# Kernel optimization log

Measured on AMD Instinct MI355X. Metric: run time of the kernel, lower is better.

Reference implementation:

```python
import jax, jax.numpy as jnp
import numpy as np

B, C, H, W = 8, 512, 32, 32
N_HEADS, HEAD_DIM = 8, 64
EPS = 1e-5


def _layernorm(x, g, b):
    mu = jnp.mean(x, axis=-1, keepdims=True)
    var = jnp.mean(jnp.square(x - mu), axis=-1, keepdims=True)
    return (x - mu) * jax.lax.rsqrt(var + EPS) * g + b


def setup_inputs() -> dict:
    key = jax.random.key(0)
    ks = jax.random.split(key, 16)
    u = lambda k, shp: jax.random.uniform(k, shp, dtype=jnp.float32)
    inp = {
        "x": jax.random.normal(ks[0], (B, C, H, W), dtype=jnp.float32),
        "t": jax.random.normal(ks[1], (B,), dtype=jnp.float32),
        # attention params (torch.rand init in source)
        "K_W": u(ks[2], (N_HEADS, C, HEAD_DIM)), "K_b": u(ks[3], (N_HEADS, HEAD_DIM)),
        "Q_W": u(ks[4], (N_HEADS, C, HEAD_DIM)), "Q_b": u(ks[5], (N_HEADS, HEAD_DIM)),
        "V_W": u(ks[6], (N_HEADS, C, HEAD_DIM)), "V_b": u(ks[7], (N_HEADS, HEAD_DIM)),
        "O_W": u(ks[8], (N_HEADS, HEAD_DIM, C)), "O_b": u(ks[9], (C,)),
        # pre-attention LayerNorm
        "ln1_g": jnp.ones((C,), jnp.float32), "ln1_b": jnp.zeros((C,), jnp.float32),
        # MLP: LayerNorm -> Linear -> GELU -> Linear
        "ln2_g": jnp.ones((C,), jnp.float32), "ln2_b": jnp.zeros((C,), jnp.float32),
        "W1": jax.random.normal(ks[10], (C, C), dtype=jnp.float32) / np.sqrt(C),
        "b1": jnp.zeros((C,), jnp.float32),
        "W2": jax.random.normal(ks[11], (C, C), dtype=jnp.float32) / np.sqrt(C),
        "b2": jnp.zeros((C,), jnp.float32),
    }
    return inp


def reference(x, t, K_W, K_b, Q_W, Q_b, V_W, V_b, O_W, O_b,
              ln1_g, ln1_b, ln2_g, ln2_b, W1, b1, W2, b2):
    b, c, h, w = x.shape
    xs = x.reshape(b, c, h * w).transpose(0, 2, 1)           # b s c
    res = _layernorm(xs, ln1_g, ln1_b)
    q = jnp.einsum('bsc,ncd->bsnd', res, Q_W) + Q_b          # b s n_h h_dim
    k = jnp.einsum('bsc,ncd->bsnd', res, K_W) + K_b
    v = jnp.einsum('bsc,ncd->bsnd', res, V_W) + V_b
    scores = jnp.einsum('bsnd,btnd->bnst', q, k) / jnp.sqrt(jnp.float32(c))
    attn = jax.nn.softmax(scores, axis=-1)                   # b n_h s s
    o = jnp.einsum('bnst,btnd->bsnd', attn, v)
    out = jnp.einsum('bsnd,ndc->bsc', o, O_W) + O_b
    out = out + xs                                           # residual
    m = _layernorm(out, ln2_g, ln2_b)
    m = jax.nn.gelu(m @ W1 + b1, approximate=False) @ W2 + b2
    out = m + out
    return out.transpose(0, 2, 1).reshape(b, c, h, w)
```

## Files before the change

### kernel.cpp

```cpp
#include <hip/hip_runtime.h>
#include <math.h>

#define BB 8
#define CC 512
#define SS 1024
#define NHH 8
#define HDD 64
#define KD 512

typedef __attribute__((ext_vector_type(8))) short short8;
typedef __attribute__((ext_vector_type(4))) float f32x4;
typedef __attribute__((ext_vector_type(4))) unsigned short ushort4v;
typedef __attribute__((ext_vector_type(2))) unsigned int u32x2;

__device__ __forceinline__ unsigned short f2bf(float x) {
  union { float f; unsigned int u; } c; c.f = x;
  unsigned int r = (c.u + 0x7FFFu + ((c.u >> 16) & 1u)) >> 16;
  return (unsigned short)r;
}
__device__ __forceinline__ float b2f(unsigned short h) {
  union { unsigned int u; float f; } c; c.u = ((unsigned int)h) << 16; return c.f;
}

#define GLD_LDS(gp, lp) __builtin_amdgcn_global_load_lds( \
    (const __attribute__((address_space(1))) void*)(gp),  \
    (__attribute__((address_space(3))) void*)(lp), 16, 0, 0)

__device__ __forceinline__ float block_reduce_sum(float v) {
  __shared__ float sm[4];
  #pragma unroll
  for (int o = 32; o > 0; o >>= 1) v += __shfl_down(v, o, 64);
  if ((threadIdx.x & 63) == 0) sm[threadIdx.x >> 6] = v;
  __syncthreads();
  float r = (sm[0] + sm[1]) + (sm[2] + sm[3]);
  __syncthreads();
  return r;
}

__global__ __launch_bounds__(256) void ln1_apply(
    const float* __restrict__ x, const float2* __restrict__ mustd,
    const float* __restrict__ g, const float* __restrict__ be,
    unsigned short* __restrict__ yh, unsigned short* __restrict__ yl,
    unsigned short* __restrict__ xh, unsigned short* __restrict__ xl) {
  __shared__ float tile[32][33];
  const int b = blockIdx.z, c0 = blockIdx.y * 32, s0 = blockIdx.x * 32;
  const int tx = threadIdx.x, ty = threadIdx.y;
  const float* xb = x + ((size_t)b * CC + c0) * SS + s0;
  #pragma unroll
  for (int i = ty; i < 32; i += 8)
    tile[i][tx] = xb[(size_t)i * SS + tx];
  __syncthreads();
  const float gc = g[c0 + tx], bc = be[c0 + tx];
  #pragma unroll
  for (int i = ty; i < 32; i += 8) {
    const float2 ms = mustd[b * SS + s0 + i];
    const float v = tile[tx][i];
    const float y = (v - ms.x) * ms.y * gc + bc;
    const size_t oi = ((size_t)b * SS + s0 + i) * CC + c0 + tx;
    const unsigned short hy = f2bf(y);
    yh[oi] = hy; yl[oi] = f2bf(y - b2f(hy));
    const unsigned short hx = f2bf(v);
    xh[oi] = hx; xl[oi] = f2bf(v - b2f(hx));
  }
}

__global__ __launch_bounds__(256) void ln_bf16_k(const float* __restrict__ in,
                                                 const float* __restrict__ g,
                                                 const float* __restrict__ be,
                                                 unsigned short* __restrict__ outh) {
  size_t row = blockIdx.x;
  const float* r = in + row * CC;
  int t = threadIdx.x;
  float v0 = r[t], v1 = r[t + 256];
  float s = block_reduce_sum(v0 + v1);
  float mu = s * (1.0f / CC);
  float d0 = v0 - mu, d1 = v1 - mu;
  float vs = block_reduce_sum(d0 * d0 + d1 * d1);
  float rstd = rsqrtf(vs * (1.0f / CC) + 1e-5f);
  outh[row * CC + t]       = f2bf(d0 * rstd * g[t] + be[t]);
  outh[row * CC + t + 256] = f2bf(d1 * rstd * g[t + 256] + be[t + 256]);
}

__global__ __launch_bounds__(256) void convert_and_stats(
    const float* __restrict__ QW, const float* __restrict__ KW,
    const float* __restrict__ VW, const float* __restrict__ OW,
    const float* __restrict__ W1, const float* __restrict__ W2,
    const float* __restrict__ Qb, const float* __restrict__ Kb,
    const float* __restrict__ Vb,
    unsigned short* __restrict__ BtQKh, unsigned short* __restrict__ BtQKl,
    unsigned short* __restrict__ BtVh,
    unsigned short* __restrict__ BtOh, unsigned short* __restrict__ BtOl,
    unsigned short* __restrict__ BtW1h, unsigned short* __restrict__ BtW2h,
    float* __restrict__ qkvb,
    const float* __restrict__ x, float2* __restrict__ mustd) {
  const int bid = blockIdx.x;
  if (bid < 1536) {
    const float SCL = 0.044194173824159216f * 1.4426950408889634f;
    __shared__ float tile[32][33];
    const int bx = bid & 15, by = (bid >> 4) & 1, p = bid >> 5;
    const int wsel = p >> 3, sub = p & 7;
    const int k0 = bx * 32, d0 = by * 32;
    const int tx = threadIdx.x & 31, ty = threadIdx.x >> 5;
    const float* w; int rs; unsigned short *dh, *dl; int nbase; float mul = 1.0f;
    switch (wsel) {
      case 0:  w = QW + sub * 32768; rs = 64;  dh = BtQKh; dl = BtQKl;  nbase = sub * 64; mul = SCL; break;
      case 1:  w = KW + sub * 32768; rs = 64;  dh = BtQKh; dl = BtQKl;  nbase = 512 + sub * 64;  break;
      case 2:  w = VW + sub * 32768; rs = 64;  dh = BtVh;  dl = nullptr; nbase = sub * 64;       break;
      case 3:  w = OW + sub * 64;    rs = 512; dh = BtOh;  dl = BtOl;   nbase = sub * 64;        break;
      case 4:  w = W1 + sub * 64;    rs = 512; dh = BtW1h; dl = nullptr; nbase = sub * 64;       break;
      default: w = W2 + sub * 64;    rs = 512; dh = BtW2h; dl = nullptr; nbase = sub * 64;       break;
    }
    for (int i = ty; i < 32; i += 8)
      tile[i][tx] = w[(size_t)(k0 + i) * rs + d0 + tx];
    __syncthreads();
    for (int i = ty; i < 32; i += 8) {
      float f = tile[tx][i] * mul;
      unsigned short h = f2bf(f);
      size_t idx = (size_t)(nbase + d0 + i) * KD + k0 + tx;
      dh[idx] = h;
      if (dl) dl[idx] = f2bf(f - b2f(h));
    }
    if (bid == 0) {
      int t = threadIdx.x;
      for (int i = t; i < 1536; i += 256)
        qkvb[i] = i < 512 ? Qb[i] * SCL : (i < 1024 ? Kb[i - 512] : Vb[i - 1024]);
    }
  } else {
    const int bid2 = bid - 1536;
    const int b = bid2 >> 4, s0 = (bid2 & 15) * 64;
    const int sl = threadIdx.x & 63, cg = threadIdx.x >> 6;
    const float* xp = x + (size_t)b * CC * SS + s0 + sl;
    float ps = 0.f, pq = 0.f;
    #pragma unroll 8
    for (int i = 0; i < 128; ++i) {
      const float v = xp[(size_t)(cg * 128 + i) * SS];
      ps += v; pq += v * v;
    }
    __shared__ float sred[2][4][64];
    sred[0][cg][sl] = ps; sred[1][cg][sl] = pq;
    __syncthreads();
    if (cg == 0) {
      const float s = (sred[0][0][sl] + sred[0][1][sl]) + (sred[0][2][sl] + sred[0][3][sl]);
      const float q = (sred[1][0][sl] + sred[1][1][sl]) + (sred[1][2][sl] + sred[1][3][sl]);
      const float mu = s * (1.0f / CC);
      const float rs = rsqrtf(q * (1.0f / CC) - mu * mu + 1e-5f);
      mustd[b * SS + s0 + sl] = make_float2(mu, rs);
    }
  }
}

__global__ __launch_bounds__(256) void gemm_qkv(
    const unsigned short* __restrict__ Ah, const unsigned short* __restrict__ Al,
    const unsigned short* __restrict__ Bth, const unsigned short* __restrict__ Btl,
    const float* __restrict__ bias,
    unsigned short* __restrict__ qkh, unsigned short* __restrict__ qkl,
    unsigned short* __restrict__ vt) {
  __shared__ __align__(16) unsigned short smem[4 * 128 * 32];
  unsigned short* As = smem;
  unsigned short* Bs = smem + 2 * 128 * 32;
  const int tid = threadIdx.x;
  const int w = tid >> 6, l = tid & 63, quad = l >> 4, lm = l & 15;
  const int f = blockIdx.x, xcd = f & 7, gidx = f >> 3;
  const int n0 = (gidx >> 3) * 128;
  const int m0 = (((gidx & 7) << 3) | xcd) * 128;
  const bool splitB = n0 < 1024;
  const int wm = (w >> 1) * 64, wn = (w & 1) * 64;
  const int srow = tid >> 2;
  const int sch = (((tid & 3) ^ (srow & 3)) * 8);
  const unsigned short* Agh = Ah + (size_t)(m0 + srow) * KD + sch;
  const unsigned short* Agl = Al + (size_t)(m0 + srow) * KD + sch;
  const unsigned short* Bgh = Bth + (size_t)(n0 + srow) * KD + sch;
  const unsigned short* Bgl = Btl + (size_t)(n0 + srow) * KD + sch;
  unsigned short* Aswh = As + w * 512;
  unsigned short* Aswl = As + 4096 + w * 512;
  unsigned short* Bswh = Bs + w * 512;
  unsigned short* Bswl = Bs + 4096 + w * 512;
  const int rch = ((quad ^ (lm & 3)) * 8);
  const f32x4 fzero = {0.f, 0.f, 0.f, 0.f};
  f32x4 acc[4][4];
  #pragma unroll
  for (int i = 0; i < 4; ++i)
    #pragma unroll
    for (int j = 0; j < 4; ++j) acc[i][j] = fzero;
  for (int k0 = 0; k0 < KD; k0 += 32) {
    __syncthreads();
    GLD_LDS(Agh + k0, Aswh);
    GLD_LDS(Agh + k0 + 64 * KD, Aswh + 2048);
    GLD_LDS(Agl + k0, Aswl);
    GLD_LDS(Agl + k0 + 64 * KD, Aswl + 2048);
    GLD_LDS(Bgh + k0, Bswh);
    GLD_LDS(Bgh + k0 + 64 * KD, Bswh + 2048);
    if (splitB) {
      GLD_LDS(Bgl + k0, Bswl);
      GLD_LDS(Bgl + k0 + 64 * KD, Bswl + 2048);
    }
    __syncthreads();
    short8 afh[4], afl[4], bfh[4], bfl[4];
    #pragma unroll
    for (int i = 0; i < 4; ++i) {
      afh[i] = *(const short8*)(As + (wm + i * 16 + lm) * 32 + rch);
      afl[i] = *(const short8*)(As + 4096 + (wm + i * 16 + lm) * 32 + rch);
    }
    #pragma unroll
    for (int j = 0; j < 4; ++j)
      bfh[j] = *(const short8*)(Bs + (wn + j * 16 + lm) * 32 + rch);
    if (splitB) {
      #pragma unroll
      for (int j = 0; j < 4; ++j)
        bfl[j] = *(const short8*)(Bs + 4096 + (wn + j * 16 + lm) * 32 + rch);
      #pragma unroll
      for (int i = 0; i < 4; ++i)
        #pragma unroll
        for (int j = 0; j < 4; ++j) {
          f32x4 t = acc[i][j];
          t = __builtin_amdgcn_mfma_f32_16x16x32_bf16(afh[i], bfh[j], t, 0, 0, 0);
          t = __builtin_amdgcn_mfma_f32_16x16x32_bf16(afh[i], bfl[j], t, 0, 0, 0);
          t = __builtin_amdgcn_mfma_f32_16x16x32_bf16(afl[i], bfh[j], t, 0, 0, 0);
          acc[i][j] = t;
        }
    } else {
      #pragma unroll
      for (int i = 0; i < 4; ++i)
        #pragma unroll
        for (int j = 0; j < 4; ++j)
          acc[i][j] = __builtin_amdgcn_mfma_f32_16x16x32_bf16(afh[i], bfh[j], acc[i][j], 0, 0, 0);
    }
  }
  if (splitB) {
    #pragma unroll
    for (int i = 0; i < 4; ++i) {
      const int row = m0 + wm + i * 16 + quad * 4;
      #pragma unroll
      for (int j = 0; j < 4; ++j) {
        const int ncol = n0 + wn + j * 16 + lm;
        const float bv = bias[ncol];
        #pragma unroll
        for (int r = 0; r < 4; ++r) {
          const float xv = acc[i][j][r] + bv;
          const size_t oi = (size_t)(row + r) * 1024 + ncol;
          unsigned short h = f2bf(xv);
          qkh[oi] = h;
          qkl[oi] = f2bf(xv - b2f(h));
        }
      }
    }
  } else {
    __syncthreads();
    #pragma unroll
    for (int i = 0; i < 4; ++i) {
      const int mlb = wm + i * 16 + quad * 4;
      #pragma unroll
      for (int j = 0; j < 4; ++j) {
        const int nl = wn + j * 16 + lm;
        const float bv = bias[n0 + nl];
        ushort4v pk;
        #pragma unroll
        for (int r = 0; r < 4; ++r) pk[r] = f2bf(acc[i][j][r] + bv);
        const int chunk = ((mlb >> 3) ^ (nl & 15));
        *(ushort4v*)(smem + nl * 128 + chunk * 8 + (mlb & 7)) = pk;
      }
    }
    __syncthreads();
    const int tn = tid >> 4, tc = tid & 15;
    const int bb2 = m0 >> 10, sbase = m0 & 1023;
    #pragma unroll
    for (int pass = 0; pass < 8; ++pass) {
      const int nl = pass * 16 + tn;
      const int hh = (n0 - 1024 + nl) >> 6, dd = nl & 63;
      short8 v8 = *(const short8*)(smem + nl * 128 + ((tc ^ (nl & 15)) * 8));
      *(short8*)(vt + ((size_t)(bb2 * 8 + hh) * 64 + dd) * 1024 + sbase + tc * 8) = v8;
    }
  }
}

template<int SB, int GELU, int OUTMODE, int RESID, int TRANS>
__global__ __launch_bounds__(256) void gemm64(
    const unsigned short* __restrict__ Ah,
    const unsigned short* __restrict__ Bh, const unsigned short* __restrict__ Bl,
    const float* __restrict__ bias, const float* __restrict__ residf,
    const unsigned short* __restrict__ residh, const unsigned short* __restrict__ residl,
    unsigned short* __restrict__ outh, float* __restrict__ outf, int ldc) {
  constexpr int STAGE = (SB ? 3 : 2) * 8192;
  constexpr int TSIZE = TRANS ? 64 * 65 * 4 : 0;
  __shared__ __align__(16) unsigned char smem[STAGE > TSIZE ? STAGE : TSIZE];
  unsigned short* As  = (unsigned short*)smem;
  unsigned short* Bs  = (unsigned short*)(smem + 8192);
  unsigned short* Bls = (unsigned short*)(smem + 16384);
  float (*ttile)[65]  = (float(*)[65])smem;
  const int tid = threadIdx.x;
  const int w = tid >> 6, l = tid & 63, quad = l >> 4, lm = l & 15;
  const int f = blockIdx.x, xcd = f & 7, gidx = f >> 3;
  const int n0 = (gidx >> 4) * 64;
  const int m0 = (((gidx & 15) << 3) | xcd) * 64;
  const int wm = (w >> 1) * 32, wn = (w & 1) * 32;
  const int srow8 = tid >> 3;
  const int sch8  = ((tid & 7) ^ (srow8 & 7)) * 8;
  const unsigned short* Ag  = Ah + (size_t)(m0 + srow8) * KD + sch8;
  const unsigned short* Bg  = Bh + (size_t)(n0 + srow8) * KD + sch8;
  const unsigned short* Bgl = SB ? Bl + (size_t)(n0 + srow8) * KD + sch8 : nullptr;
  const f32x4 fzero = {0.f, 0.f, 0.f, 0.f};
  f32x4 acc[2][2];
  #pragma unroll
  for (int i = 0; i < 2; ++i)
    #pragma unroll
    for (int j = 0; j < 2; ++j) acc[i][j] = fzero;
  for (int k0 = 0; k0 < KD; k0 += 64) {
    __syncthreads();
    GLD_LDS(Ag + k0, As + w * 512);
    GLD_LDS(Ag + k0 + 32 * KD, As + 2048 + w * 512);
    GLD_LDS(Bg + k0, Bs + w * 512);
    GLD_LDS(Bg + k0 + 32 * KD, Bs + 2048 + w * 512);
    if constexpr (SB) {
      GLD_LDS(Bgl + k0, Bls + w * 512);
      GLD_LDS(Bgl + k0 + 32 * KD, Bls + 2048 + w * 512);
    }
    __syncthreads();
    #pragma unroll
    for (int ks = 0; ks < 2; ++ks) {
      const int kc = ((ks * 4 + quad) ^ (lm & 7)) * 8;
      short8 af[2], bfh[2], bfl[2];
      #pragma unroll
      for (int i = 0; i < 2; ++i)
        af[i] = *(const short8*)(As + (wm + i * 16 + lm) * 64 + kc);
      #pragma unroll
      for (int j = 0; j < 2; ++j)
        bfh[j] = *(const short8*)(Bs + (wn + j * 16 + lm) * 64 + kc);
      if constexpr (SB) {
        #pragma unroll
        for (int j = 0; j < 2; ++j)
          bfl[j] = *(const short8*)(Bls + (wn + j * 16 + lm) * 64 + kc);
      }
      #pragma unroll
      for (int i = 0; i < 2; ++i)
        #pragma unroll
        for (int j = 0; j < 2; ++j) {
          f32x4 t = acc[i][j];
          t = __builtin_amdgcn_mfma_f32_16x16x32_bf16(af[i], bfh[j], t, 0, 0, 0);
          if constexpr (SB)
            t = __builtin_amdgcn_mfma_f32_16x16x32_bf16(af[i], bfl[j], t, 0, 0, 0);
          acc[i][j] = t;
        }
    }
  }
  if constexpr (TRANS) __syncthreads();
  #pragma unroll
  for (int i = 0; i < 2; ++i) {
    const int row = m0 + wm + i * 16 + quad * 4;
    #pragma unroll
    for (int j = 0; j < 2; ++j) {
      const int col = n0 + wn + j * 16 + lm;
      const float bv = bias[col];
      #pragma unroll
      for (int r = 0; r < 4; ++r) {
        float x = acc[i][j][r] + bv;
        if (GELU) x = 0.5f * x * (1.0f + erff(x * 0.70710678118654752f));
        const size_t ri = (size_t)(row + r) * CC + col;
        if (RESID == 1) x += residf[ri];
        if (RESID == 2) x += b2f(residh[ri]) + b2f(residl[ri]);
        if constexpr (TRANS) {
          ttile[wm + i * 16 + quad * 4 + r][wn + j * 16 + lm] = x;
        } else {
          const size_t oi = (size_t)(row + r) * ldc + col;
          if (OUTMODE == 0) outf[oi] = x;
          else outh[oi] = f2bf(x);
        }
      }
    }
  }
  if constexpr (TRANS) {
    __syncthreads();
    const int bi = m0 >> 10, s0 = m0 & 1023;
    const int s = tid & 63;
    #pragma unroll
    for (int c0 = 0; c0 < 64; c0 += 4) {
      const int col = c0 + (tid >> 6);
      outf[(size_t)(bi * 512 + n0 + col) * 1024 + s0 + s] = ttile[s][col];
    }
  }
}

__global__ __launch_bounds__(256) void attn_mfma(
    const unsigned short* __restrict__ QKh, const unsigned short* __restrict__ QKl,
    const unsigned short* __restrict__ Vt, unsigned short* __restrict__ Oh) {
  __shared__ __align__(16) unsigned short Ksh[64 * 64], Ksl[64 * 64];
  __shared__ __align__(16) unsigned short Vts[64 * 64];
  __shared__ __align__(16) unsigned short Pts[4][16 * 64];
  const int f = blockIdx.x, xcd = f & 7, gidx = f >> 3;
  const int bh = (xcd << 3) | (gidx >> 4);
  const int q0 = (gidx & 15) * 64, h = bh & 7, b = bh >> 3;
  const int tid = threadIdx.x, w = tid >> 6, l = tid & 63, quad = l >> 4, lm = l & 15;
  const int LDQ = 2 * CC;
  const size_t qkbase = (size_t)b * SS * LDQ;
  const int srow8 = tid >> 3;
  const int sch8  = ((tid & 7) ^ (srow8 & 7)) * 8;
  const unsigned short* Vg = Vt + ((size_t)(b * 8 + h) * 64 + srow8) * 1024 + sch8;
  short8 qh[2], ql[2];
  {
    const size_t qo = qkbase + (size_t)(q0 + w * 16 + lm) * LDQ + h * 64 + quad * 8;
    qh[0] = *(const short8*)(QKh + qo);
    qh[1] = *(const short8*)(QKh + qo + 32);
    ql[0] = *(const short8*)(QKl + qo);
    ql[1] = *(const short8*)(QKl + qo + 32);
  }
  const f32x4 fzero = {0.f, 0.f, 0.f, 0.f};
  float m = -1e30f, lsum = 0.f;
  f32x4 oacc[4];
  #pragma unroll
  for (int j = 0; j < 4; ++j) oacc[j] = fzero;
  unsigned char* Pb = (unsigned char*)(Pts[w]);
  const int pwbase = lm * 128 + ((quad & 1) << 3);
  const int prbase = lm * 128;
  for (int kt = 0; kt < SS; kt += 64) {
    __syncthreads();
    {
      const unsigned short* kg  = QKh + qkbase + (size_t)(kt + srow8) * LDQ + CC + h * 64 + sch8;
      const unsigned short* kgl = QKl + qkbase + (size_t)(kt + srow8) * LDQ + CC + h * 64 + sch8;
      GLD_LDS(kg, Ksh + w * 512);
      GLD_LDS(kg + 32 * LDQ, Ksh + 2048 + w * 512);
      GLD_LDS(kgl, Ksl + w * 512);
      GLD_LDS(kgl + 32 * LDQ, Ksl + 2048 + w * 512);
      GLD_LDS(Vg + kt, Vts + w * 512);
      GLD_LDS(Vg + kt + 32 * 1024, Vts + 2048 + w * 512);
    }
    __syncthreads();
    f32x4 sc[4];
    {
      const int kc = (quad ^ (lm & 7)) * 8;
      #pragma unroll
      for (int j = 0; j < 4; ++j) {
        short8 kh = *(const short8*)(Ksh + (j * 16 + lm) * 64 + kc);
        short8 kl = *(const short8*)(Ksl + (j * 16 + lm) * 64 + kc);
        f32x4 t = __builtin_amdgcn_mfma_f32_16x16x32_bf16(kh, qh[0], fzero, 0, 0, 0);
        t = __builtin_amdgcn_mfma_f32_16x16x32_bf16(kl, qh[0], t, 0, 0, 0);
        t = __builtin_amdgcn_mfma_f32_16x16x32_bf16(kh, ql[0], t, 0, 0, 0);
        sc[j] = t;
      }
    }
    {
      const int kc = ((4 + quad) ^ (lm & 7)) * 8;
      #pragma unroll
      for (int j = 0; j < 4; ++j) {
        short8 kh = *(const short8*)(Ksh + (j * 16 + lm) * 64 + kc);
        short8 kl = *(const short8*)(Ksl + (j * 16 + lm) * 64 + kc);
        f32x4 t = sc[j];
        t = __builtin_amdgcn_mfma_f32_16x16x32_bf16(kh, qh[1], t, 0, 0, 0);
        t = __builtin_amdgcn_mfma_f32_16x16x32_bf16(kl, qh[1], t, 0, 0, 0);
        t = __builtin_amdgcn_mfma_f32_16x16x32_bf16(kh, ql[1], t, 0, 0, 0);
        sc[j] = t;
      }
    }
    float mt0 = fmaxf(fmaxf(sc[0][0], sc[0][1]), fmaxf(sc[0][2], sc[0][3]));
    float mt1 = fmaxf(fmaxf(sc[1][0], sc[1][1]), fmaxf(sc[1][2], sc[1][3]));
    float mt2 = fmaxf(fmaxf(sc[2][0], sc[2][1]), fmaxf(sc[2][2], sc[2][3]));
    float mt3 = fmaxf(fmaxf(sc[3][0], sc[3][1]), fmaxf(sc[3][2], sc[3][3]));
    float mt = fmaxf(fmaxf(mt0, mt1), fmaxf(mt2, mt3));
    mt = fmaxf(mt, __shfl_xor(mt, 16, 64));
    mt = fmaxf(mt, __shfl_xor(mt, 32, 64));
    const float mnew = fmaxf(m, mt);
    if (__any(mnew > m)) {
      const float alpha = exp2f(m - mnew);
      m = mnew;
      lsum *= alpha;
      #pragma unroll
      for (int j = 0; j < 4; ++j)
        #pragma unroll
        for (int r = 0; r < 4; ++r) oacc[j][r] *= alpha;
    }
    float ls = 0.f;
    #pragma unroll
    for (int j = 0; j < 4; ++j)
      #pragma unroll
      for (int r = 0; r < 4; ++r) {
        sc[j][r] = exp2f(sc[j][r] - m);
        ls += sc[j][r];
      }
    ls += __shfl_xor(ls, 16, 64);
    ls += __shfl_xor(ls, 32, 64);
    lsum += ls;
    #pragma unroll
    for (int j = 0; j < 4; ++j) {
      union { float f; unsigned int u; } c0, c1, c2, c3;
      c0.f = sc[j][0]; c1.f = sc[j][1]; c2.f = sc[j][2]; c3.f = sc[j][3];
      u32x2 pk;
      pk[0] = __builtin_amdgcn_perm(c1.u, c0.u, 0x07060302u);
      pk[1] = __builtin_amdgcn_perm(c3.u, c2.u, 0x07060302u);
      const int slot = ((j << 1) | (quad >> 1)) ^ (lm & 7);
      *(u32x2*)(Pb + pwbase + (slot << 4)) = pk;
    }
    #pragma unroll
    for (int st = 0; st < 2; ++st) {
      short8 pf = *(const short8*)(Pb + prbase + ((((st << 2) | quad) ^ (lm & 7)) << 4));
      const int kc = ((st * 4 + quad) ^ (lm & 7)) * 8;
      #pragma unroll
      for (int j = 0; j < 4; ++j) {
        short8 vv = *(const short8*)(Vts + (j * 16 + lm) * 64 + kc);
        oacc[j] = __builtin_amdgcn_mfma_f32_16x16x32_bf16(vv, pf, oacc[j], 0, 0, 0);
      }
    }
  }
  const float inv = 1.f / lsum;
  const size_t obase =
      (size_t)b * SS * CC + (size_t)(q0 + w * 16 + lm) * CC + h * 64 + quad * 4;
  #pragma unroll
  for (int j = 0; j < 4; ++j) {
    ushort4v pk;
    #pragma unroll
    for (int r = 0; r < 4; ++r) pk[r] = f2bf(oacc[j][r] * inv);
    *(ushort4v*)(Oh + obase + j * 16) = pk;
  }
}

extern "C" void kernel_launch(void* const* d_in, const int* in_sizes, int n_in,
                              void* d_out, int out_size, void* d_ws, size_t ws_size,
                              hipStream_t stream) {
  const float* x    = (const float*)d_in[0];
  const float* K_W  = (const float*)d_in[2];
  const float* K_b  = (const float*)d_in[3];
  const float* Q_W  = (const float*)d_in[4];
  const float* Q_b  = (const float*)d_in[5];
  const float* V_W  = (const float*)d_in[6];
  const float* V_b  = (const float*)d_in[7];
  const float* O_W  = (const float*)d_in[8];
  const float* O_b  = (const float*)d_in[9];
  const float* ln1g = (const float*)d_in[10];
  const float* ln1b = (const float*)d_in[11];
  const float* ln2g = (const float*)d_in[12];
  const float* ln2b = (const float*)d_in[13];
  const float* W1   = (const float*)d_in[14];
  const float* b1   = (const float*)d_in[15];
  const float* W2   = (const float*)d_in[16];
  const float* b2   = (const float*)d_in[17];
  float* out = (float*)d_out;

  unsigned char* ws = (unsigned char*)d_ws;
  const size_t MB = 1u << 20;
  unsigned short* qkh   = (unsigned short*)(ws);
  unsigned short* qkl   = (unsigned short*)(ws + 16 * MB);
  unsigned short* vt    = (unsigned short*)(ws + 32 * MB);
  unsigned short* ln1h  = (unsigned short*)(ws + 40 * MB);
  unsigned short* ln1l  = (unsigned short*)(ws + 48 * MB);
  unsigned short* xsh   = (unsigned short*)(ws + 56 * MB);
  unsigned short* xsl   = (unsigned short*)(ws + 64 * MB);
  unsigned short* oh    = ln1h;
  float* out1           = (float*)(ws + 72 * MB);
  unsigned short* ln2h  = qkh;
  unsigned short* geluh = (unsigned short*)(ws + 8 * MB);
  unsigned short* BtAll = (unsigned short*)(ws + 88 * MB);
  unsigned short* BtQKh = BtAll;
  unsigned short* BtVh  = BtAll + 1024 * 512;
  unsigned short* BtQKl = BtVh + 512 * 512;
  unsigned short* BtOh  = BtQKl + 1024 * 512;
  unsigned short* BtOl  = BtOh + 512 * 512;
  unsigned short* BtW1h = BtOl + 512 * 512;
  unsigned short* BtW2h = BtW1h + 512 * 512;
  float* qkvb           = (float*)(BtW2h + 512 * 512);
  float2* mustd         = (float2*)(ws + 96 * MB);

  dim3 tb32(32, 8);
  convert_and_stats<<<1536 + 128, 256, 0, stream>>>(
      Q_W, K_W, V_W, O_W, W1, W2, Q_b, K_b, V_b,
      BtQKh, BtQKl, BtVh, BtOh, BtOl, BtW1h, BtW2h, qkvb, x, mustd);
  ln1_apply<<<dim3(SS / 32, CC / 32, BB), tb32, 0, stream>>>(
      x, mustd, ln1g, ln1b, ln1h, ln1l, xsh, xsl);
  gemm_qkv<<<768, 256, 0, stream>>>(
      ln1h, ln1l, BtAll, BtQKl, qkvb, qkh, qkl, vt);
  attn_mfma<<<1024, 256, 0, stream>>>(qkh, qkl, vt, oh);
  gemm64<1, 0, 0, 2, 0><<<1024, 256, 0, stream>>>(
      oh, BtOh, BtOl, O_b, nullptr, xsh, xsl, nullptr, out1, CC);
  ln_bf16_k<<<BB * SS, 256, 0, stream>>>(out1, ln2g, ln2b, ln2h);
  gemm64<0, 1, 1, 0, 0><<<1024, 256, 0, stream>>>(
      ln2h, BtW1h, nullptr, b1, nullptr, nullptr, nullptr, geluh, nullptr, CC);
  gemm64<0, 0, 0, 1, 1><<<1024, 256, 0, stream>>>(
      geluh, BtW2h, nullptr, b2, out1, nullptr, nullptr, nullptr, out, CC);
}
```

Before: 264.3 us.

## Register-prefetch next K/V tile in attention loop and raise MFMA priority

The attention kernel used direct global-to-LDS loads, with each K/V tile loaded and waited on before compute. It now loads the next tile into registers during the current tile's compute and writes them to LDS at the start of the next iteration, overlapping global latency with the MFMA work. The MFMA sections are also wrapped in s_setprio(1)/(0) to favour matrix issue across waves. This costs extra VGPRs, which may lower occupancy, and adds a register-to-LDS store pass in place of the direct LDS load path.

```diff
diff --git a/kernel.cpp b/kernel.cpp
--- a/kernel.cpp
+++ b/kernel.cpp
@@ -393,7 +393,10 @@
   const size_t qkbase = (size_t)b * SS * LDQ;
   const int srow8 = tid >> 3;
   const int sch8  = ((tid & 7) ^ (srow8 & 7)) * 8;
-  const unsigned short* Vg = Vt + ((size_t)(b * 8 + h) * 64 + srow8) * 1024 + sch8;
+  const unsigned short* Vg  = Vt + ((size_t)(b * 8 + h) * 64 + srow8) * 1024 + sch8;
+  const unsigned short* kgh = QKh + qkbase + (size_t)srow8 * LDQ + CC + h * 64 + sch8;
+  const unsigned short* kgl = QKl + qkbase + (size_t)srow8 * LDQ + CC + h * 64 + sch8;
+  const int lofs = w * 512 + l * 8;
   short8 qh[2], ql[2];
   {
     const size_t qo = qkbase + (size_t)(q0 + w * 16 + lm) * LDQ + h * 64 + quad * 8;
@@ -410,20 +413,32 @@
   unsigned char* Pb = (unsigned char*)(Pts[w]);
   const int pwbase = lm * 128 + ((quad & 1) << 3);
   const int prbase = lm * 128;
+  short8 s0h = *(const short8*)(kgh);
+  short8 s1h = *(const short8*)(kgh + (size_t)32 * LDQ);
+  short8 s0l = *(const short8*)(kgl);
+  short8 s1l = *(const short8*)(kgl + (size_t)32 * LDQ);
+  short8 s0v = *(const short8*)(Vg);
+  short8 s1v = *(const short8*)(Vg + 32 * 1024);
   for (int kt = 0; kt < SS; kt += 64) {
     __syncthreads();
+    *(short8*)(Ksh + lofs)        = s0h;
+    *(short8*)(Ksh + 2048 + lofs) = s1h;
+    *(short8*)(Ksl + lofs)        = s0l;
+    *(short8*)(Ksl + 2048 + lofs) = s1l;
+    *(short8*)(Vts + lofs)        = s0v;
+    *(short8*)(Vts + 2048 + lofs) = s1v;
+    __syncthreads();
     {
-      const unsigned short* kg  = QKh + qkbase + (size_t)(kt + srow8) * LDQ + CC + h * 64 + sch8;
-      const unsigned short* kgl = QKl + qkbase + (size_t)(kt + srow8) * LDQ + CC + h * 64 + sch8;
-      GLD_LDS(kg, Ksh + w * 512);
-      GLD_LDS(kg + 32 * LDQ, Ksh + 2048 + w * 512);
-      GLD_LDS(kgl, Ksl + w * 512);
-      GLD_LDS(kgl + 32 * LDQ, Ksl + 2048 + w * 512);
-      GLD_LDS(Vg + kt, Vts + w * 512);
-      GLD_LDS(Vg + kt + 32 * 1024, Vts + 2048 + w * 512);
-    }
-    __syncthreads();
+      const int ktn = (kt + 64) & (SS - 1);
+      s0h = *(const short8*)(kgh + (size_t)ktn * LDQ);
+      s1h = *(const short8*)(kgh + (size_t)(ktn + 32) * LDQ);
+      s0l = *(const short8*)(kgl + (size_t)ktn * LDQ);
+      s1l = *(const short8*)(kgl + (size_t)(ktn + 32) * LDQ);
+      s0v = *(const short8*)(Vg + ktn);
+      s1v = *(const short8*)(Vg + ktn + 32 * 1024);
+    }
     f32x4 sc[4];
+    __builtin_amdgcn_s_setprio(1);
     {
       const int kc = (quad ^ (lm & 7)) * 8;
       #pragma unroll
@@ -449,6 +464,7 @@
         sc[j] = t;
       }
     }
+    __builtin_amdgcn_s_setprio(0);
     float mt0 = fmaxf(fmaxf(sc[0][0], sc[0][1]), fmaxf(sc[0][2], sc[0][3]));
     float mt1 = fmaxf(fmaxf(sc[1][0], sc[1][1]), fmaxf(sc[1][2], sc[1][3]));
     float mt2 = fmaxf(fmaxf(sc[2][0], sc[2][1]), fmaxf(sc[2][2], sc[2][3]));
@@ -487,6 +503,7 @@
       const int slot = ((j << 1) | (quad >> 1)) ^ (lm & 7);
       *(u32x2*)(Pb + pwbase + (slot << 4)) = pk;
     }
+    __builtin_amdgcn_s_setprio(1);
     #pragma unroll
     for (int st = 0; st < 2; ++st) {
       short8 pf = *(const short8*)(Pb + prbase + ((((st << 2) | quad) ^ (lm & 7)) << 4));
@@ -497,6 +514,7 @@
         oacc[j] = __builtin_amdgcn_mfma_f32_16x16x32_bf16(vv, pf, oacc[j], 0, 0, 0);
       }
     }
+    __builtin_amdgcn_s_setprio(0);
   }
   const float inv = 1.f / lsum;
   const size_t obase =
```

New measurement: 260.3 us. No clear change (-1.5%).
